# Kernel tuning notes

Hardware: AMD Instinct MI355X
Metric: run time of the kernel (lower is better)

Reference implementation:

```python
import jax, jax.numpy as jnp
import numpy as np

N, NH, G, SEG, RATIO = 500000, 128, 10000, 25, 2
P = G * SEG            # 250000 pos samples
PN = P * RATIO         # 500000 neg samples


def setup_inputs() -> dict:
    key = jax.random.key(0)
    k1, k2, k3, k4, k5, k6 = jax.random.split(key, 6)
    return {
        "embedding": jax.random.normal(k1, (N, NH), jnp.float32),
        "embedding_": jax.random.normal(k2, (N, NH), jnp.float32),
        "grid_sizes": jnp.full((G,), SEG, dtype=jnp.int64 if jax.config.jax_enable_x64 else jnp.int32),
        "pos_samples": jax.random.randint(k3, (P,), 0, N),
        "neg_samples": jax.random.randint(k4, (PN,), 0, N),
        "Wi": jax.random.normal(k5, (NH, NH), jnp.float32) * (1.0 / np.sqrt(NH)),
        "bi": jnp.zeros((NH,), jnp.float32),
        "Wk": jax.random.normal(k6, (NH, NH), jnp.float32) * (1.0 / np.sqrt(NH)),  # Bilinear weight [1,nh,nh] squeezed
        "bk": jnp.zeros((1,), jnp.float32),
    }


def reference(embedding, embedding_, grid_sizes, pos_samples, neg_samples, Wi, bi, Wk, bk):
    Pl = pos_samples.shape[0]
    Gl = grid_sizes.shape[0]
    ratio = neg_samples.shape[0] // Pl  # static int

    # segment ids: grid index repeated grid_sizes[i] times (sum == P)
    seg_ids = jnp.repeat(jnp.arange(Gl), grid_sizes, total_repeat_length=Pl)

    # f_i on embedding_ , gather pos, segment-mean per grid
    emb_ = embedding_ @ Wi.T + bi                      # [N, nh]
    pos_e_ = emb_[pos_samples]                         # [P, nh]
    seg_sum = jax.ops.segment_sum(pos_e_, seg_ids, num_segments=Gl)
    grid_embed = seg_sum / grid_sizes[:, None].astype(seg_sum.dtype)  # [G, nh]

    # f_i on embedding, gather pos/neg samples
    emb = embedding @ Wi.T + bi
    pos_embed = emb[pos_samples]                       # [P, nh]
    neg_embed = emb[neg_samples]                       # [P*ratio, nh]

    # broadcast grid embedding back to per-sample rows
    pos_grid = grid_embed[seg_ids]                     # [P, nh]
    neg_seg_ids = jnp.repeat(jnp.arange(Gl), grid_sizes * ratio,
                             total_repeat_length=Pl * ratio)
    neg_grid = grid_embed[neg_seg_ids]                 # [P*ratio, nh]

    # bilinear score: x1 W x2 + b (out features = 1, squeezed)
    pos_logits = jnp.einsum('nd,de,ne->n', pos_embed, Wk, pos_grid) + bk[0]
    neg_logits = jnp.einsum('nd,de,ne->n', neg_embed, Wk, neg_grid) + bk[0]
    return jnp.concatenate((pos_logits, neg_logits))
```

## Files before the change

kernel.cpp:

```cpp
#include <hip/hip_runtime.h>

#define NH 128

__global__ void scan_kernel(const int* __restrict__ gs, int* __restrict__ c, int G) {
    __shared__ int part[1024];
    int t = threadIdx.x;
    int chunk = (G + 1023) >> 10;
    int b = t * chunk;
    int e = min(b + chunk, G);
    int s = 0;
    for (int i = b; i < e; ++i) s += gs[i];
    part[t] = s;
    __syncthreads();
    for (int off = 1; off < 1024; off <<= 1) {
        int val = (t >= off) ? part[t - off] : 0;
        __syncthreads();
        part[t] += val;
        __syncthreads();
    }
    int excl = (t == 0) ? 0 : part[t - 1];
    for (int i = b; i < e; ++i) { c[i] = excl; excl += gs[i]; }
    if (t == 1023) c[G] = part[1023];
}

__global__ void matA_kernel(const float* __restrict__ Wk, const float* __restrict__ Wi,
                            const float* __restrict__ bi,
                            float* __restrict__ A, float* __restrict__ u) {
    int tid = blockIdx.x * blockDim.x + threadIdx.x;
    int e = tid >> 7, d = tid & (NH - 1);
    float acc = 0.f;
    for (int f = 0; f < NH; ++f) acc += Wk[e * NH + f] * Wi[f * NH + d];
    A[e * NH + d] = acc;
    if (tid < NH) {
        float s = 0.f;
        for (int f = 0; f < NH; ++f) s += Wk[tid * NH + f] * bi[f];
        u[tid] = s;
    }
}

__global__ void matB_kernel(const float* __restrict__ Wi, const float* __restrict__ bi,
                            const float* __restrict__ bk,
                            const float* __restrict__ A, const float* __restrict__ u,
                            float* __restrict__ Bt, float* __restrict__ v,
                            float* __restrict__ w, float* __restrict__ s0) {
    int tid = blockIdx.x * blockDim.x + threadIdx.x;
    int i = tid & (NH - 1);
    int j = tid >> 7;
    float acc = 0.f;
    for (int e = 0; e < NH; ++e) acc += Wi[e * NH + i] * A[e * NH + j];
    Bt[j * NH + i] = acc;
    if (tid < NH) {
        float s = 0.f;
        for (int e = 0; e < NH; ++e) s += Wi[e * NH + tid] * u[e];
        v[tid] = s;
    } else if (tid < 2 * NH) {
        int jj = tid - NH;
        float s = 0.f;
        for (int e = 0; e < NH; ++e) s += bi[e] * A[e * NH + jj];
        w[jj] = s;
    }
    if (tid == 0) {
        float s = 0.f;
        for (int e = 0; e < NH; ++e) s += bi[e] * u[e];
        s0[0] = s + bk[0];
    }
}

__global__ void seg_mean_kernel(const float* __restrict__ emb_, const int* __restrict__ pos,
                                const int* __restrict__ c, float* __restrict__ M, int G) {
    __shared__ float smf[8 * NH];
    int g = blockIdx.x;
    int t = threadIdx.x;
    int lane = t & 31, slot = t >> 5;
    int b = c[g], e = c[g + 1];
    float4 acc = make_float4(0.f, 0.f, 0.f, 0.f);
    for (int r = b + slot; r < e; r += 8) {
        int row = pos[r];
        const float4 a = ((const float4*)(emb_ + (size_t)row * NH))[lane];
        acc.x += a.x; acc.y += a.y; acc.z += a.z; acc.w += a.w;
    }
    ((float4*)(smf + slot * NH))[lane] = acc;
    __syncthreads();
    if (t < NH) {
        float s = 0.f;
#pragma unroll
        for (int s2 = 0; s2 < 8; ++s2) s += smf[s2 * NH + t];
        float cnt = (float)max(e - b, 1);
        M[(size_t)g * NH + t] = s / cnt;
    }
}

#define SPB 8
__global__ void q_kernel(const float* __restrict__ M, const float* __restrict__ Bt,
                         const float* __restrict__ v, const float* __restrict__ w,
                         const float* __restrict__ s0,
                         float* __restrict__ Q, float* __restrict__ C2, int G) {
    __shared__ float m[SPB][NH];
    __shared__ float red[SPB][2];
    int d = threadIdx.x;
    int g0 = blockIdx.x * SPB;
    int ns = min(SPB, G - g0);
    for (int s = 0; s < SPB; ++s)
        m[s][d] = (s < ns) ? M[(size_t)(g0 + s) * NH + d] : 0.f;
    __syncthreads();

    float q[SPB];
#pragma unroll
    for (int s = 0; s < SPB; ++s) q[s] = 0.f;
    for (int f = 0; f < NH; ++f) {
        float bt = Bt[f * NH + d];
#pragma unroll
        for (int s = 0; s < SPB; ++s) q[s] += bt * m[s][f];
    }
    float vd = v[d], wd = w[d], s00 = s0[0];
    for (int s = 0; s < ns; ++s)
        Q[(size_t)(g0 + s) * NH + d] = q[s] + vd;

    int lane = d & 63, wv = d >> 6;
    for (int s = 0; s < SPB; ++s) {
        float tval = wd * m[s][d];
        for (int off = 32; off; off >>= 1) tval += __shfl_xor(tval, off);
        if (lane == 0) red[s][wv] = tval;
    }
    __syncthreads();
    if (d < SPB && d < ns) C2[g0 + d] = red[d][0] + red[d][1] + s00;
}

__global__ void logits_kernel(const float* __restrict__ emb, const int* __restrict__ pos,
                              const int* __restrict__ neg, const int* __restrict__ c,
                              const float* __restrict__ Q, const float* __restrict__ C2,
                              float* __restrict__ out, int P, int ratio) {
    __shared__ float qs[NH];
    __shared__ int idx[512];
    int g = blockIdx.x;
    int t = threadIdx.x;
    if (t < NH) qs[t] = Q[(size_t)g * NH + t];
    int pb = c[g], pe = c[g + 1];
    int np = pe - pb;
    int nb = pb * ratio;
    int tot = np + np * ratio;
    int lane = t & 31, slot = t >> 5;
    __syncthreads();
    float4 qr = ((const float4*)qs)[lane];
    float c2 = C2[g];

    for (int k0 = 0; k0 < tot; k0 += 512) {
        int kend = min(tot - k0, 512);
        __syncthreads();
        for (int k = t; k < kend; k += 256) {
            int kk = k0 + k;
            idx[k] = (kk < np) ? pos[pb + kk] : neg[nb + kk - np];
        }
        __syncthreads();
        for (int k = slot; k < kend; k += 8) {
            int kk = k0 + k;
            int row = idx[k];
            const float4 a = ((const float4*)(emb + (size_t)row * NH))[lane];
            float val = a.x * qr.x + a.y * qr.y + a.z * qr.z + a.w * qr.w;
#pragma unroll
            for (int off = 16; off; off >>= 1) val += __shfl_xor(val, off, 32);
            if (lane == 0) {
                int o = (kk < np) ? (pb + kk) : (P + nb + kk - np);
                out[o] = val + c2;
            }
        }
    }
}

extern "C" void kernel_launch(void* const* d_in, const int* in_sizes, int n_in,
                              void* d_out, int out_size, void* d_ws, size_t ws_size,
                              hipStream_t stream) {
    const float* embedding  = (const float*)d_in[0];
    const float* embedding_ = (const float*)d_in[1];
    const int*   grid_sizes = (const int*)d_in[2];
    const int*   pos        = (const int*)d_in[3];
    const int*   neg        = (const int*)d_in[4];
    const float* Wi         = (const float*)d_in[5];
    const float* bi         = (const float*)d_in[6];
    const float* Wk         = (const float*)d_in[7];
    const float* bk         = (const float*)d_in[8];

    int G = in_sizes[2];
    int P = in_sizes[3];
    int PN = in_sizes[4];
    int ratio = PN / P;

    char* ws = (char*)d_ws;
    size_t off = 0;
    auto alloc = [&](size_t bytes) {
        void* p = ws + off;
        off += (bytes + 255) & ~(size_t)255;
        return p;
    };
    int*   c   = (int*)  alloc((size_t)(G + 1) * sizeof(int));
    float* A   = (float*)alloc(NH * NH * sizeof(float));
    float* u   = (float*)alloc(NH * sizeof(float));
    float* Bt  = (float*)alloc(NH * NH * sizeof(float));
    float* v   = (float*)alloc(NH * sizeof(float));
    float* w   = (float*)alloc(NH * sizeof(float));
    float* s0  = (float*)alloc(sizeof(float));
    float* Q   = (float*)alloc((size_t)G * NH * sizeof(float));
    float* C2  = (float*)alloc((size_t)G * sizeof(float));
    float* M   = (float*)alloc((size_t)G * NH * sizeof(float));
    (void)ws_size; (void)n_in; (void)out_size;

    hipLaunchKernelGGL(scan_kernel, dim3(1), dim3(1024), 0, stream, grid_sizes, c, G);
    hipLaunchKernelGGL(matA_kernel, dim3((NH * NH) / 256), dim3(256), 0, stream,
                       Wk, Wi, bi, A, u);
    hipLaunchKernelGGL(matB_kernel, dim3((NH * NH) / 256), dim3(256), 0, stream,
                       Wi, bi, bk, A, u, Bt, v, w, s0);
    hipLaunchKernelGGL(seg_mean_kernel, dim3(G), dim3(256), 0, stream,
                       embedding_, pos, c, M, G);
    hipLaunchKernelGGL(q_kernel, dim3((G + SPB - 1) / SPB), dim3(NH), 0, stream,
                       M, Bt, v, w, s0, Q, C2, G);
    hipLaunchKernelGGL(logits_kernel, dim3(G), dim3(256), 0, stream,
                       embedding, pos, neg, c, Q, C2, (float*)d_out, P, ratio);
}
```

Baseline: 539.1 us.

## Fuse segment-mean, query projection and logits into one per-grid kernel

Merges the segment-mean, Q/C2 projection and logits kernels into a single 512-thread per-grid kernel that keeps the mean and the query vector in shared memory, so the M, Q and C2 global buffers are no longer written and read back. It issues the first gathered embedding rows into registers before the Bt matvec so those loads overlap that computation. It also merges the scan and matA setup kernels into one launch. The fused kernel recomputes the 128x128 Bt matvec per grid in every block and needs more registers and shared memory per block, which could lower occupancy.

```diff
diff --git a/kernel.cpp b/kernel.cpp
--- a/kernel.cpp
+++ b/kernel.cpp
@@ -1,40 +1,43 @@
 #include <hip/hip_runtime.h>
 
 #define NH 128
-
-__global__ void scan_kernel(const int* __restrict__ gs, int* __restrict__ c, int G) {
-    __shared__ int part[1024];
-    int t = threadIdx.x;
-    int chunk = (G + 1023) >> 10;
-    int b = t * chunk;
-    int e = min(b + chunk, G);
-    int s = 0;
-    for (int i = b; i < e; ++i) s += gs[i];
-    part[t] = s;
-    __syncthreads();
-    for (int off = 1; off < 1024; off <<= 1) {
-        int val = (t >= off) ? part[t - off] : 0;
+#define SLOTS 16
+#define PF 5
+
+__global__ void setup1_kernel(const int* __restrict__ gs, int* __restrict__ c, int G,
+                              const float* __restrict__ Wk, const float* __restrict__ Wi,
+                              const float* __restrict__ bi,
+                              float* __restrict__ A, float* __restrict__ u) {
+    if (blockIdx.x == 0) {
+        __shared__ int part[1024];
+        int t = threadIdx.x;
+        int chunk = (G + 1023) >> 10;
+        int b = t * chunk;
+        int e = min(b + chunk, G);
+        int s = 0;
+        for (int i = b; i < e; ++i) s += gs[i];
+        part[t] = s;
         __syncthreads();
-        part[t] += val;
-        __syncthreads();
-    }
-    int excl = (t == 0) ? 0 : part[t - 1];
-    for (int i = b; i < e; ++i) { c[i] = excl; excl += gs[i]; }
-    if (t == 1023) c[G] = part[1023];
-}
-
-__global__ void matA_kernel(const float* __restrict__ Wk, const float* __restrict__ Wi,
-                            const float* __restrict__ bi,
-                            float* __restrict__ A, float* __restrict__ u) {
-    int tid = blockIdx.x * blockDim.x + threadIdx.x;
-    int e = tid >> 7, d = tid & (NH - 1);
-    float acc = 0.f;
-    for (int f = 0; f < NH; ++f) acc += Wk[e * NH + f] * Wi[f * NH + d];
-    A[e * NH + d] = acc;
-    if (tid < NH) {
-        float s = 0.f;
-        for (int f = 0; f < NH; ++f) s += Wk[tid * NH + f] * bi[f];
-        u[tid] = s;
+        for (int off = 1; off < 1024; off <<= 1) {
+            int val = (t >= off) ? part[t - off] : 0;
+            __syncthreads();
+            part[t] += val;
+            __syncthreads();
+        }
+        int excl = (t == 0) ? 0 : part[t - 1];
+        for (int i = b; i < e; ++i) { c[i] = excl; excl += gs[i]; }
+        if (t == 1023) c[G] = part[1023];
+    } else {
+        int tid = (blockIdx.x - 1) * 1024 + threadIdx.x;
+        int e = tid >> 7, d = tid & (NH - 1);
+        float acc = 0.f;
+        for (int f = 0; f < NH; ++f) acc += Wk[e * NH + f] * Wi[f * NH + d];
+        A[e * NH + d] = acc;
+        if (tid < NH) {
+            float s = 0.f;
+            for (int f = 0; f < NH; ++f) s += Wk[tid * NH + f] * bi[f];
+            u[tid] = s;
+        }
     }
 }
 
@@ -66,96 +69,80 @@
     }
 }
 
-__global__ void seg_mean_kernel(const float* __restrict__ emb_, const int* __restrict__ pos,
-                                const int* __restrict__ c, float* __restrict__ M, int G) {
-    __shared__ float smf[8 * NH];
+__global__ __launch_bounds__(512, 6)
+void mega_kernel(const float* __restrict__ emb, const float* __restrict__ emb_,
+                 const int* __restrict__ pos, const int* __restrict__ neg,
+                 const int* __restrict__ c, const float* __restrict__ Bt,
+                 const float* __restrict__ v, const float* __restrict__ w,
+                 const float* __restrict__ s0, float* __restrict__ out,
+                 int P, int ratio) {
+    __shared__ float smf[SLOTS * NH];
+    __shared__ float m[NH];
+    __shared__ float qp[4][NH];
+    __shared__ float qs[NH];
+    __shared__ float redc[2];
+
     int g = blockIdx.x;
     int t = threadIdx.x;
     int lane = t & 31, slot = t >> 5;
-    int b = c[g], e = c[g + 1];
-    float4 acc = make_float4(0.f, 0.f, 0.f, 0.f);
-    for (int r = b + slot; r < e; r += 8) {
-        int row = pos[r];
-        const float4 a = ((const float4*)(emb_ + (size_t)row * NH))[lane];
-        acc.x += a.x; acc.y += a.y; acc.z += a.z; acc.w += a.w;
-    }
-    ((float4*)(smf + slot * NH))[lane] = acc;
-    __syncthreads();
-    if (t < NH) {
-        float s = 0.f;
-#pragma unroll
-        for (int s2 = 0; s2 < 8; ++s2) s += smf[s2 * NH + t];
-        float cnt = (float)max(e - b, 1);
-        M[(size_t)g * NH + t] = s / cnt;
-    }
-}
-
-#define SPB 8
-__global__ void q_kernel(const float* __restrict__ M, const float* __restrict__ Bt,
-                         const float* __restrict__ v, const float* __restrict__ w,
-                         const float* __restrict__ s0,
-                         float* __restrict__ Q, float* __restrict__ C2, int G) {
-    __shared__ float m[SPB][NH];
-    __shared__ float red[SPB][2];
-    int d = threadIdx.x;
-    int g0 = blockIdx.x * SPB;
-    int ns = min(SPB, G - g0);
-    for (int s = 0; s < SPB; ++s)
-        m[s][d] = (s < ns) ? M[(size_t)(g0 + s) * NH + d] : 0.f;
-    __syncthreads();
-
-    float q[SPB];
-#pragma unroll
-    for (int s = 0; s < SPB; ++s) q[s] = 0.f;
-    for (int f = 0; f < NH; ++f) {
-        float bt = Bt[f * NH + d];
-#pragma unroll
-        for (int s = 0; s < SPB; ++s) q[s] += bt * m[s][f];
-    }
-    float vd = v[d], wd = w[d], s00 = s0[0];
-    for (int s = 0; s < ns; ++s)
-        Q[(size_t)(g0 + s) * NH + d] = q[s] + vd;
-
-    int lane = d & 63, wv = d >> 6;
-    for (int s = 0; s < SPB; ++s) {
-        float tval = wd * m[s][d];
-        for (int off = 32; off; off >>= 1) tval += __shfl_xor(tval, off);
-        if (lane == 0) red[s][wv] = tval;
-    }
-    __syncthreads();
-    if (d < SPB && d < ns) C2[g0 + d] = red[d][0] + red[d][1] + s00;
-}
-
-__global__ void logits_kernel(const float* __restrict__ emb, const int* __restrict__ pos,
-                              const int* __restrict__ neg, const int* __restrict__ c,
-                              const float* __restrict__ Q, const float* __restrict__ C2,
-                              float* __restrict__ out, int P, int ratio) {
-    __shared__ float qs[NH];
-    __shared__ int idx[512];
-    int g = blockIdx.x;
-    int t = threadIdx.x;
-    if (t < NH) qs[t] = Q[(size_t)g * NH + t];
+
     int pb = c[g], pe = c[g + 1];
     int np = pe - pb;
     int nb = pb * ratio;
     int tot = np + np * ratio;
-    int lane = t & 31, slot = t >> 5;
-    __syncthreads();
+
+    float4 acc = make_float4(0.f, 0.f, 0.f, 0.f);
+    for (int r = pb + slot; r < pe; r += SLOTS) {
+        int row = pos[r];
+        const float4 a = ((const float4*)(emb_ + (size_t)row * NH))[lane];
+        acc.x += a.x; acc.y += a.y; acc.z += a.z; acc.w += a.w;
+    }
+    ((float4*)(smf + slot * NH))[lane] = acc;
+    __syncthreads();
+    if (t < NH) {
+        float s = 0.f;
+#pragma unroll
+        for (int k = 0; k < SLOTS; ++k) s += smf[k * NH + t];
+        m[t] = s / (float)max(np, 1);
+    }
+    __syncthreads();
+
+    float4 areg[PF];
+#pragma unroll
+    for (int i = 0; i < PF; ++i) {
+        int kk = slot + i * SLOTS;
+        if (kk < tot) {
+            int row = (kk < np) ? pos[pb + kk] : neg[nb + kk - np];
+            areg[i] = ((const float4*)(emb + (size_t)row * NH))[lane];
+        }
+    }
+
+    {
+        int d = t & (NH - 1);
+        int quarter = t >> 7;
+        int f0 = quarter * 32;
+        float p = 0.f;
+#pragma unroll 8
+        for (int f = f0; f < f0 + 32; ++f) p += Bt[f * NH + d] * m[f];
+        qp[quarter][d] = p;
+    }
+    __syncthreads();
+    if (t < NH) {
+        qs[t] = qp[0][t] + qp[1][t] + qp[2][t] + qp[3][t] + v[t];
+        float val = w[t] * m[t];
+#pragma unroll
+        for (int off = 32; off; off >>= 1) val += __shfl_xor(val, off, 64);
+        if ((t & 63) == 0) redc[t >> 6] = val;
+    }
+    __syncthreads();
+    float c2 = redc[0] + redc[1] + s0[0];
     float4 qr = ((const float4*)qs)[lane];
-    float c2 = C2[g];
-
-    for (int k0 = 0; k0 < tot; k0 += 512) {
-        int kend = min(tot - k0, 512);
-        __syncthreads();
-        for (int k = t; k < kend; k += 256) {
-            int kk = k0 + k;
-            idx[k] = (kk < np) ? pos[pb + kk] : neg[nb + kk - np];
-        }
-        __syncthreads();
-        for (int k = slot; k < kend; k += 8) {
-            int kk = k0 + k;
-            int row = idx[k];
-            const float4 a = ((const float4*)(emb + (size_t)row * NH))[lane];
+
+#pragma unroll
+    for (int i = 0; i < PF; ++i) {
+        int kk = slot + i * SLOTS;
+        if (kk < tot) {
+            float4 a = areg[i];
             float val = a.x * qr.x + a.y * qr.y + a.z * qr.z + a.w * qr.w;
 #pragma unroll
             for (int off = 16; off; off >>= 1) val += __shfl_xor(val, off, 32);
@@ -163,6 +150,17 @@
                 int o = (kk < np) ? (pb + kk) : (P + nb + kk - np);
                 out[o] = val + c2;
             }
+        }
+    }
+    for (int kk = slot + PF * SLOTS; kk < tot; kk += SLOTS) {
+        int row = (kk < np) ? pos[pb + kk] : neg[nb + kk - np];
+        const float4 a = ((const float4*)(emb + (size_t)row * NH))[lane];
+        float val = a.x * qr.x + a.y * qr.y + a.z * qr.z + a.w * qr.w;
+#pragma unroll
+        for (int off = 16; off; off >>= 1) val += __shfl_xor(val, off, 32);
+        if (lane == 0) {
+            int o = (kk < np) ? (pb + kk) : (P + nb + kk - np);
+            out[o] = val + c2;
         }
     }
 }
@@ -199,20 +197,13 @@
     float* v   = (float*)alloc(NH * sizeof(float));
     float* w   = (float*)alloc(NH * sizeof(float));
     float* s0  = (float*)alloc(sizeof(float));
-    float* Q   = (float*)alloc((size_t)G * NH * sizeof(float));
-    float* C2  = (float*)alloc((size_t)G * sizeof(float));
-    float* M   = (float*)alloc((size_t)G * NH * sizeof(float));
     (void)ws_size; (void)n_in; (void)out_size;
 
-    hipLaunchKernelGGL(scan_kernel, dim3(1), dim3(1024), 0, stream, grid_sizes, c, G);
-    hipLaunchKernelGGL(matA_kernel, dim3((NH * NH) / 256), dim3(256), 0, stream,
-                       Wk, Wi, bi, A, u);
+    hipLaunchKernelGGL(setup1_kernel, dim3(1 + (NH * NH) / 1024), dim3(1024), 0, stream,
+                       grid_sizes, c, G, Wk, Wi, bi, A, u);
     hipLaunchKernelGGL(matB_kernel, dim3((NH * NH) / 256), dim3(256), 0, stream,
                        Wi, bi, bk, A, u, Bt, v, w, s0);
-    hipLaunchKernelGGL(seg_mean_kernel, dim3(G), dim3(256), 0, stream,
-                       embedding_, pos, c, M, G);
-    hipLaunchKernelGGL(q_kernel, dim3((G + SPB - 1) / SPB), dim3(NH), 0, stream,
-                       M, Bt, v, w, s0, Q, C2, G);
-    hipLaunchKernelGGL(logits_kernel, dim3(G), dim3(256), 0, stream,
-                       embedding, pos, neg, c, Q, C2, (float*)d_out, P, ratio);
-}
+    hipLaunchKernelGGL(mega_kernel, dim3(G), dim3(512), 0, stream,
+                       embedding, embedding_, pos, neg, c, Bt, v, w, s0,
+                       (float*)d_out, P, ratio);
+}
```

Measured after the change: 563.2 us. 4.5% more time.

## Flatten logits into grid-stride sample loop and wave-per-segment mean with segment ids

Applied to the files above, without the earlier changes.

Merges the scan and first weight-product kernels into one launch. Rewrites the segment-mean kernel to process one segment per wavefront with shuffled indices and 8 unrolled gathers, while also emitting per-sample segment ids. The logits kernel becomes a grid-stride loop over all samples with 4 gathers in flight per group, looking up Q rows via segment ids and a magic-number division for negatives. This aims to raise memory-level parallelism and even out load balance, at the cost of extra Q-row gathers and a segid write/read.

```diff
diff --git a/kernel.cpp b/kernel.cpp
--- a/kernel.cpp
+++ b/kernel.cpp
@@ -2,39 +2,40 @@
 
 #define NH 128
 
-__global__ void scan_kernel(const int* __restrict__ gs, int* __restrict__ c, int G) {
-    __shared__ int part[1024];
-    int t = threadIdx.x;
-    int chunk = (G + 1023) >> 10;
-    int b = t * chunk;
-    int e = min(b + chunk, G);
-    int s = 0;
-    for (int i = b; i < e; ++i) s += gs[i];
-    part[t] = s;
-    __syncthreads();
-    for (int off = 1; off < 1024; off <<= 1) {
-        int val = (t >= off) ? part[t - off] : 0;
+__global__ void setup1_kernel(const int* __restrict__ gs, int* __restrict__ c, int G,
+                              const float* __restrict__ Wk, const float* __restrict__ Wi,
+                              const float* __restrict__ bi,
+                              float* __restrict__ A, float* __restrict__ u) {
+    if (blockIdx.x == 0) {
+        __shared__ int part[1024];
+        int t = threadIdx.x;
+        int chunk = (G + 1023) >> 10;
+        int b = t * chunk;
+        int e = min(b + chunk, G);
+        int s = 0;
+        for (int i = b; i < e; ++i) s += gs[i];
+        part[t] = s;
         __syncthreads();
-        part[t] += val;
-        __syncthreads();
-    }
-    int excl = (t == 0) ? 0 : part[t - 1];
-    for (int i = b; i < e; ++i) { c[i] = excl; excl += gs[i]; }
-    if (t == 1023) c[G] = part[1023];
-}
-
-__global__ void matA_kernel(const float* __restrict__ Wk, const float* __restrict__ Wi,
-                            const float* __restrict__ bi,
-                            float* __restrict__ A, float* __restrict__ u) {
-    int tid = blockIdx.x * blockDim.x + threadIdx.x;
-    int e = tid >> 7, d = tid & (NH - 1);
-    float acc = 0.f;
-    for (int f = 0; f < NH; ++f) acc += Wk[e * NH + f] * Wi[f * NH + d];
-    A[e * NH + d] = acc;
-    if (tid < NH) {
-        float s = 0.f;
-        for (int f = 0; f < NH; ++f) s += Wk[tid * NH + f] * bi[f];
-        u[tid] = s;
+        for (int off = 1; off < 1024; off <<= 1) {
+            int val = (t >= off) ? part[t - off] : 0;
+            __syncthreads();
+            part[t] += val;
+            __syncthreads();
+        }
+        int excl = (t == 0) ? 0 : part[t - 1];
+        for (int i = b; i < e; ++i) { c[i] = excl; excl += gs[i]; }
+        if (t == 1023) c[G] = part[1023];
+    } else {
+        int tid = (blockIdx.x - 1) * 1024 + threadIdx.x;
+        int e = tid >> 7, d = tid & (NH - 1);
+        float acc = 0.f;
+        for (int f = 0; f < NH; ++f) acc += Wk[e * NH + f] * Wi[f * NH + d];
+        A[e * NH + d] = acc;
+        if (tid < NH) {
+            float s = 0.f;
+            for (int f = 0; f < NH; ++f) s += Wk[tid * NH + f] * bi[f];
+            u[tid] = s;
+        }
     }
 }
 
@@ -66,27 +67,44 @@
     }
 }
 
-__global__ void seg_mean_kernel(const float* __restrict__ emb_, const int* __restrict__ pos,
-                                const int* __restrict__ c, float* __restrict__ M, int G) {
-    __shared__ float smf[8 * NH];
-    int g = blockIdx.x;
-    int t = threadIdx.x;
-    int lane = t & 31, slot = t >> 5;
-    int b = c[g], e = c[g + 1];
-    float4 acc = make_float4(0.f, 0.f, 0.f, 0.f);
-    for (int r = b + slot; r < e; r += 8) {
-        int row = pos[r];
-        const float4 a = ((const float4*)(emb_ + (size_t)row * NH))[lane];
-        acc.x += a.x; acc.y += a.y; acc.z += a.z; acc.w += a.w;
-    }
-    ((float4*)(smf + slot * NH))[lane] = acc;
-    __syncthreads();
-    if (t < NH) {
-        float s = 0.f;
-#pragma unroll
-        for (int s2 = 0; s2 < 8; ++s2) s += smf[s2 * NH + t];
-        float cnt = (float)max(e - b, 1);
-        M[(size_t)g * NH + t] = s / cnt;
+#define MCH 8
+__global__ __launch_bounds__(256, 8)
+void seg_mean_kernel(const float* __restrict__ emb_, const int* __restrict__ pos,
+                     const int* __restrict__ c, float* __restrict__ M,
+                     int* __restrict__ segid, int G) {
+    int wave  = (blockIdx.x * blockDim.x + threadIdx.x) >> 6;
+    int lane  = threadIdx.x & 63;
+    int nwave = (gridDim.x * blockDim.x) >> 6;
+    for (int g = wave; g < G; g += nwave) {
+        int pb = c[g], pe = c[g + 1];
+        int np = pe - pb;
+        float2 acc = make_float2(0.f, 0.f);
+        for (int r0 = 0; r0 < np; r0 += 64) {
+            int nr = min(64, np - r0);
+            int idxv = 0;
+            if (lane < nr) {
+                idxv = pos[pb + r0 + lane];
+                segid[pb + r0 + lane] = g;
+            }
+            int r = 0;
+            for (; r + MCH <= nr; r += MCH) {
+                float2 a[MCH];
+#pragma unroll
+                for (int j = 0; j < MCH; ++j) {
+                    int row = __shfl(idxv, r + j, 64);
+                    a[j] = ((const float2*)(emb_ + (size_t)row * NH))[lane];
+                }
+#pragma unroll
+                for (int j = 0; j < MCH; ++j) { acc.x += a[j].x; acc.y += a[j].y; }
+            }
+            for (; r < nr; ++r) {
+                int row = __shfl(idxv, r, 64);
+                float2 a = ((const float2*)(emb_ + (size_t)row * NH))[lane];
+                acc.x += a.x; acc.y += a.y;
+            }
+        }
+        float cnt = (float)max(np, 1);
+        ((float2*)(M + (size_t)g * NH))[lane] = make_float2(acc.x / cnt, acc.y / cnt);
     }
 }
 
@@ -126,43 +144,51 @@
     if (d < SPB && d < ns) C2[g0 + d] = red[d][0] + red[d][1] + s00;
 }
 
-__global__ void logits_kernel(const float* __restrict__ emb, const int* __restrict__ pos,
-                              const int* __restrict__ neg, const int* __restrict__ c,
-                              const float* __restrict__ Q, const float* __restrict__ C2,
-                              float* __restrict__ out, int P, int ratio) {
-    __shared__ float qs[NH];
-    __shared__ int idx[512];
-    int g = blockIdx.x;
-    int t = threadIdx.x;
-    if (t < NH) qs[t] = Q[(size_t)g * NH + t];
-    int pb = c[g], pe = c[g + 1];
-    int np = pe - pb;
-    int nb = pb * ratio;
-    int tot = np + np * ratio;
-    int lane = t & 31, slot = t >> 5;
-    __syncthreads();
-    float4 qr = ((const float4*)qs)[lane];
-    float c2 = C2[g];
-
-    for (int k0 = 0; k0 < tot; k0 += 512) {
-        int kend = min(tot - k0, 512);
-        __syncthreads();
-        for (int k = t; k < kend; k += 256) {
-            int kk = k0 + k;
-            idx[k] = (kk < np) ? pos[pb + kk] : neg[nb + kk - np];
-        }
-        __syncthreads();
-        for (int k = slot; k < kend; k += 8) {
-            int kk = k0 + k;
-            int row = idx[k];
-            const float4 a = ((const float4*)(emb + (size_t)row * NH))[lane];
-            float val = a.x * qr.x + a.y * qr.y + a.z * qr.z + a.w * qr.w;
+#define U 4
+__global__ __launch_bounds__(256, 6)
+void logits_kernel(const float* __restrict__ emb, const int* __restrict__ pos,
+                   const int* __restrict__ neg, const int* __restrict__ segid,
+                   const float* __restrict__ Q, const float* __restrict__ C2,
+                   float* __restrict__ out, int P, int PN,
+                   unsigned long long magic) {
+    int tot = P + PN;
+    int gid  = (blockIdx.x * blockDim.x + threadIdx.x) >> 5;
+    int lane = threadIdx.x & 31;
+    int ngrp = (gridDim.x * blockDim.x) >> 5;
+    long long stride = (long long)ngrp * U;
+
+    for (long long base = (long long)gid * U; base < tot; base += stride) {
+        int kk[U], row[U], sid[U];
+#pragma unroll
+        for (int j = 0; j < U; ++j) {
+            int k = (int)base + j;
+            int k2 = (k < tot) ? k : (tot - 1);
+            kk[j] = k2;
+            if (k2 < P) {
+                row[j] = pos[k2];
+                sid[j] = segid[k2];
+            } else {
+                int jn = k2 - P;
+                row[j] = neg[jn];
+                int jp = (int)(((unsigned long long)(unsigned)jn * magic) >> 42);
+                sid[j] = segid[jp];
+            }
+        }
+        float4 a[U], q[U];
+        float c2v[U];
+#pragma unroll
+        for (int j = 0; j < U; ++j) {
+            a[j]   = ((const float4*)(emb + (size_t)row[j] * NH))[lane];
+            q[j]   = ((const float4*)(Q   + (size_t)sid[j] * NH))[lane];
+            c2v[j] = C2[sid[j]];
+        }
+#pragma unroll
+        for (int j = 0; j < U; ++j) {
+            float val = a[j].x * q[j].x + a[j].y * q[j].y
+                      + a[j].z * q[j].z + a[j].w * q[j].w;
 #pragma unroll
             for (int off = 16; off; off >>= 1) val += __shfl_xor(val, off, 32);
-            if (lane == 0) {
-                int o = (kk < np) ? (pb + kk) : (P + nb + kk - np);
-                out[o] = val + c2;
-            }
+            if (lane == 0 && base + j < tot) out[kk[j]] = val + c2v[j];
         }
     }
 }
@@ -183,7 +209,9 @@
     int G = in_sizes[2];
     int P = in_sizes[3];
     int PN = in_sizes[4];
-    int ratio = PN / P;
+    int ratio = (P > 0) ? (PN / P) : 1;
+    if (ratio < 1) ratio = 1;
+    unsigned long long magic = (((unsigned long long)1 << 42) + ratio - 1) / (unsigned long long)ratio;
 
     char* ws = (char*)d_ws;
     size_t off = 0;
@@ -192,27 +220,28 @@
         off += (bytes + 255) & ~(size_t)255;
         return p;
     };
-    int*   c   = (int*)  alloc((size_t)(G + 1) * sizeof(int));
-    float* A   = (float*)alloc(NH * NH * sizeof(float));
-    float* u   = (float*)alloc(NH * sizeof(float));
-    float* Bt  = (float*)alloc(NH * NH * sizeof(float));
-    float* v   = (float*)alloc(NH * sizeof(float));
-    float* w   = (float*)alloc(NH * sizeof(float));
-    float* s0  = (float*)alloc(sizeof(float));
-    float* Q   = (float*)alloc((size_t)G * NH * sizeof(float));
-    float* C2  = (float*)alloc((size_t)G * sizeof(float));
-    float* M   = (float*)alloc((size_t)G * NH * sizeof(float));
+    int*   c     = (int*)  alloc((size_t)(G + 1) * sizeof(int));
+    float* A     = (float*)alloc(NH * NH * sizeof(float));
+    float* u     = (float*)alloc(NH * sizeof(float));
+    float* Bt    = (float*)alloc(NH * NH * sizeof(float));
+    float* v     = (float*)alloc(NH * sizeof(float));
+    float* w     = (float*)alloc(NH * sizeof(float));
+    float* s0    = (float*)alloc(sizeof(float));
+    float* M     = (float*)alloc((size_t)G * NH * sizeof(float));
+    float* Q     = (float*)alloc((size_t)G * NH * sizeof(float));
+    float* C2    = (float*)alloc((size_t)G * sizeof(float));
+    int*   segid = (int*)  alloc((size_t)P * sizeof(int));
     (void)ws_size; (void)n_in; (void)out_size;
 
-    hipLaunchKernelGGL(scan_kernel, dim3(1), dim3(1024), 0, stream, grid_sizes, c, G);
-    hipLaunchKernelGGL(matA_kernel, dim3((NH * NH) / 256), dim3(256), 0, stream,
-                       Wk, Wi, bi, A, u);
+    hipLaunchKernelGGL(setup1_kernel, dim3(1 + (NH * NH) / 1024), dim3(1024), 0, stream,
+                       grid_sizes, c, G, Wk, Wi, bi, A, u);
     hipLaunchKernelGGL(matB_kernel, dim3((NH * NH) / 256), dim3(256), 0, stream,
                        Wi, bi, bk, A, u, Bt, v, w, s0);
-    hipLaunchKernelGGL(seg_mean_kernel, dim3(G), dim3(256), 0, stream,
-                       embedding_, pos, c, M, G);
+    int smblocks = (G + 3) / 4;
+    hipLaunchKernelGGL(seg_mean_kernel, dim3(smblocks), dim3(256), 0, stream,
+                       embedding_, pos, c, M, segid, G);
     hipLaunchKernelGGL(q_kernel, dim3((G + SPB - 1) / SPB), dim3(NH), 0, stream,
                        M, Bt, v, w, s0, Q, C2, G);
-    hipLaunchKernelGGL(logits_kernel, dim3(G), dim3(256), 0, stream,
-                       embedding, pos, neg, c, Q, C2, (float*)d_out, P, ratio);
-}
+    hipLaunchKernelGGL(logits_kernel, dim3(2048), dim3(256), 0, stream,
+                       embedding, pos, neg, segid, Q, C2, (float*)d_out, P, PN, magic);
+}
```

After: 528.5 us. 1.02x faster.
